# Performance work log

Hardware: AMD Instinct MI355X
Metric: run time of the kernel (lower is better)

Reference implementation:

```python
import jax, jax.numpy as jnp
import numpy as np

N_SRC = 100000
E = 300000
D = 256
HEADS = 8
D_K = D // HEADS
N_EXPERTS = 5


def setup_inputs() -> dict:
    key = jax.random.key(0)
    kx, ki, ke, kw, kb = jax.random.split(key, 5)
    x = jax.random.normal(kx, (N_SRC, D), dtype=jnp.float32)
    index = jax.random.randint(ki, (E,), 0, N_SRC)
    # disjoint routing masks: each output row handled by exactly one of 5 linears
    expert_id = jax.random.randint(ke, (E,), 0, N_EXPERTS)
    masks = expert_id[None, :] == jnp.arange(N_EXPERTS)[:, None]  # [5, E] bool
    # learned params: 5 independent Linear(D, D) layers (torch layout: y = x @ W.T + b)
    bound = 1.0 / np.sqrt(D)
    W = jax.random.uniform(kw, (N_EXPERTS, D, D), minval=-bound, maxval=bound, dtype=jnp.float32)
    b = jax.random.uniform(kb, (N_EXPERTS, D), minval=-bound, maxval=bound, dtype=jnp.float32)
    return {"x": x, "W": W, "b": b, "index": index, "masks": masks}


def reference(x, W, b, index, masks):
    # gather source rows for every output slot: [E, D]
    xi = x[index]
    out = jnp.zeros((xi.shape[0], D), dtype=x.dtype)
    # sequential masked overwrite matches torch's output[mask] = ... semantics
    for i in range(N_EXPERTS):
        yi = xi @ W[i].T + b[i]  # [E, D]
        out = jnp.where(masks[i][:, None], yi, out)
    return out.reshape(xi.shape[0], HEADS, D_K)
```

## Files before the change

kernel.cpp:

```cpp
#include <hip/hip_runtime.h>
#include <hip/hip_bf16.h>

#define E_TOT   300000
#define D_DIM   256
#define N_EXP   5
#define BM      64
#define LDK     264
#define NB_CNT  ((E_TOT + 255) / 256)
#define MAX_TILES (E_TOT / BM + N_EXP)
#define CHUNK   8
#define NCHUNK  ((NB_CNT + CHUNK - 1) / CHUNK)

typedef __attribute__((ext_vector_type(8))) short bf16x8;
typedef __attribute__((ext_vector_type(4))) float f32x4;

__device__ inline unsigned short f2bf(float f) {
  union { float f; unsigned u; } v; v.f = f;
  unsigned u = v.u;
  u += 0x7FFFu + ((u >> 16) & 1u);
  return (unsigned short)(u >> 16);
}

__global__ void detect_kernel(const unsigned int* __restrict__ m32, int* __restrict__ hdr) {
  int tid = blockIdx.x * blockDim.x + threadIdx.x;
  const int n = (N_EXP * E_TOT) / 4;
  unsigned s = 0;
  for (int i = tid; i < n; i += gridDim.x * blockDim.x) {
    unsigned v = m32[i];
    s += (v & 0xFFu) + ((v >> 8) & 0xFFu) + ((v >> 16) & 0xFFu) + ((v >> 24) & 0xFFu);
  }
  for (int o = 32; o > 0; o >>= 1) s += __shfl_down(s, o);
  if ((threadIdx.x & 63) == 0 && s) atomicAdd(&hdr[5], (int)s);
}

__device__ inline int get_expert(const void* masks, int e, bool is_u8) {
  if (is_u8) {
    const unsigned char* m = (const unsigned char*)masks;
#pragma unroll
    for (int i = 0; i < N_EXP; ++i) if (m[(size_t)i * E_TOT + e]) return i;
  } else {
    const int* m = (const int*)masks;
#pragma unroll
    for (int i = 0; i < N_EXP; ++i) if (m[(size_t)i * E_TOT + e]) return i;
  }
  return 0;
}

__global__ void count_kernel(const void* __restrict__ masks, const int* __restrict__ hdr,
                             int* __restrict__ blockCounts) {
  __shared__ int wc[4][N_EXP];
  bool is_u8 = (hdr[5] == E_TOT);
  int e = blockIdx.x * blockDim.x + threadIdx.x;
  int ex = (e < E_TOT) ? get_expert(masks, e, is_u8) : -1;
  int w = threadIdx.x >> 6, lane = threadIdx.x & 63;
#pragma unroll
  for (int i = 0; i < N_EXP; ++i) {
    unsigned long long bal = __ballot(ex == i);
    if (lane == 0) wc[w][i] = __popcll(bal);
  }
  __syncthreads();
  if (threadIdx.x < N_EXP)
    blockCounts[blockIdx.x * N_EXP + threadIdx.x] =
        wc[0][threadIdx.x] + wc[1][threadIdx.x] + wc[2][threadIdx.x] + wc[3][threadIdx.x];
}

__global__ void scan_kernel(const int* __restrict__ blockCounts, int* __restrict__ hdr,
                            int* __restrict__ blockBase) {
  __shared__ int cs[NCHUNK][N_EXP];
  __shared__ int cp[NCHUNK][N_EXP];
  int t = threadIdx.x;
  if (t < NCHUNK) {
    int s[N_EXP] = {0, 0, 0, 0, 0};
    int b1 = min((t + 1) * CHUNK, NB_CNT);
    for (int b = t * CHUNK; b < b1; ++b)
#pragma unroll
      for (int i = 0; i < N_EXP; ++i) s[i] += blockCounts[b * N_EXP + i];
#pragma unroll
    for (int i = 0; i < N_EXP; ++i) cs[t][i] = s[i];
  }
  __syncthreads();
  if (t < N_EXP) {
    int run = 0;
    for (int c = 0; c < NCHUNK; ++c) { cp[c][t] = run; run += cs[c][t]; }
    hdr[t] = run;
  }
  __syncthreads();
  if (t == 0) {
    int run = 0;
    for (int i = 0; i < N_EXP; ++i) { hdr[8 + i] = run; run += hdr[i]; }
  }
  __syncthreads();
  if (t < NCHUNK) {
    int r[N_EXP];
#pragma unroll
    for (int i = 0; i < N_EXP; ++i) r[i] = hdr[8 + i] + cp[t][i];
    int b1 = min((t + 1) * CHUNK, NB_CNT);
    for (int b = t * CHUNK; b < b1; ++b)
#pragma unroll
      for (int i = 0; i < N_EXP; ++i) { blockBase[b * N_EXP + i] = r[i]; r[i] += blockCounts[b * N_EXP + i]; }
  }
}

__global__ void scatter_kernel(const void* __restrict__ masks, const int* __restrict__ hdr,
                               const int* __restrict__ blockBase, int* __restrict__ perm) {
  __shared__ int wc[4][N_EXP];
  __shared__ int wo[4][N_EXP];
  __shared__ int bb[N_EXP];
  bool is_u8 = (hdr[5] == E_TOT);
  int e = blockIdx.x * blockDim.x + threadIdx.x;
  int ex = (e < E_TOT) ? get_expert(masks, e, is_u8) : -1;
  int w = threadIdx.x >> 6, lane = threadIdx.x & 63;
  unsigned long long myBal = 0;
#pragma unroll
  for (int i = 0; i < N_EXP; ++i) {
    unsigned long long bal = __ballot(ex == i);
    if (lane == 0) wc[w][i] = __popcll(bal);
    if (ex == i) myBal = bal;
  }
  if (threadIdx.x < N_EXP) bb[threadIdx.x] = blockBase[blockIdx.x * N_EXP + threadIdx.x];
  __syncthreads();
  if (threadIdx.x < 4 * N_EXP) {
    int ww = threadIdx.x / N_EXP, ii = threadIdx.x % N_EXP;
    int s = 0;
    for (int p = 0; p < ww; ++p) s += wc[p][ii];
    wo[ww][ii] = s;
  }
  __syncthreads();
  if (ex >= 0) {
    int rank = __popcll(myBal & ((1ull << lane) - 1ull));
    perm[bb[ex] + wo[w][ex] + rank] = e;
  }
}

__global__ void convw_kernel(const float* __restrict__ W, unsigned short* __restrict__ Wbf) {
  int i = blockIdx.x * blockDim.x + threadIdx.x;
  float4 v = ((const float4*)W)[i];
  ushort4 o;
  o.x = f2bf(v.x); o.y = f2bf(v.y); o.z = f2bf(v.z); o.w = f2bf(v.w);
  ((ushort4*)Wbf)[i] = o;
}

template <bool PRE>
__launch_bounds__(256, 4)
__global__ void gemm_kernel(const float* __restrict__ x, const float* __restrict__ W,
                            const unsigned short* __restrict__ Wbf,
                            const float* __restrict__ bias, const int* __restrict__ index,
                            const int* __restrict__ hdr, const int* __restrict__ perm,
                            float* __restrict__ out) {
  __shared__ __align__(16) unsigned short lA[BM * LDK];
  __shared__ int srcRow[BM];
  __shared__ int outRow[BM];

  int t = (int)blockIdx.x;
  int ex = -1, trow = 0, cnt = 0, accT = 0;
#pragma unroll
  for (int i = 0; i < N_EXP; ++i) {
    int c = hdr[i];
    int nt = (c + BM - 1) / BM;
    if (ex < 0 && t < accT + nt) { ex = i; trow = t - accT; cnt = c; }
    accT += nt;
  }
  if (ex < 0) return;
  int row0 = hdr[8 + ex] + trow * BM;
  int rows = min(BM, cnt - trow * BM);

  const int tt = threadIdx.x;
  if (tt < BM) {
    int rr = min(tt, rows - 1);
    int e = perm[row0 + rr];
    outRow[tt] = e;
    srcRow[tt] = index[e];
  }
  __syncthreads();

#pragma unroll
  for (int i = 0; i < 16; ++i) {
    int lin = i * 256 + tt;
    int r = lin >> 6;
    int c4 = lin & 63;
    const float4 v = ((const float4*)(x + (size_t)srcRow[r] * D_DIM))[c4];
    ushort4 o;
    o.x = f2bf(v.x); o.y = f2bf(v.y); o.z = f2bf(v.z); o.w = f2bf(v.w);
    *(ushort4*)&lA[r * LDK + c4 * 4] = o;
  }
  __syncthreads();

  const int w = tt >> 6, lane = tt & 63, quad = lane >> 4, l16 = lane & 15;

  f32x4 acc[4][4];
#pragma unroll
  for (int mt = 0; mt < 4; ++mt)
#pragma unroll
    for (int nt = 0; nt < 4; ++nt) acc[mt][nt] = (f32x4){0.f, 0.f, 0.f, 0.f};

#pragma unroll
  for (int ks = 0; ks < 8; ++ks) {
    int k0 = ks * 32 + quad * 8;
    bf16x8 a[4], b[4];
#pragma unroll
    for (int mt = 0; mt < 4; ++mt)
      a[mt] = *(const bf16x8*)&lA[(mt * 16 + l16) * LDK + k0];
#pragma unroll
    for (int nt = 0; nt < 4; ++nt) {
      int col = w * 64 + nt * 16 + l16;
      if (PRE) {
        b[nt] = *(const bf16x8*)&Wbf[((size_t)ex * D_DIM + col) * D_DIM + k0];
      } else {
        const float* wp = W + ((size_t)ex * D_DIM + col) * D_DIM + k0;
        float4 v0 = ((const float4*)wp)[0];
        float4 v1 = ((const float4*)wp)[1];
        bf16x8 bb;
        bb[0] = (short)f2bf(v0.x); bb[1] = (short)f2bf(v0.y);
        bb[2] = (short)f2bf(v0.z); bb[3] = (short)f2bf(v0.w);
        bb[4] = (short)f2bf(v1.x); bb[5] = (short)f2bf(v1.y);
        bb[6] = (short)f2bf(v1.z); bb[7] = (short)f2bf(v1.w);
        b[nt] = bb;
      }
    }
#pragma unroll
    for (int mt = 0; mt < 4; ++mt)
#pragma unroll
      for (int nt = 0; nt < 4; ++nt)
        acc[mt][nt] = __builtin_amdgcn_mfma_f32_16x16x32_bf16(a[mt], b[nt], acc[mt][nt], 0, 0, 0);
  }

#pragma unroll
  for (int nt = 0; nt < 4; ++nt) {
    int col = w * 64 + nt * 16 + l16;
    float bv = bias[ex * D_DIM + col];
#pragma unroll
    for (int mt = 0; mt < 4; ++mt) {
#pragma unroll
      for (int r = 0; r < 4; ++r) {
        int rl = mt * 16 + quad * 4 + r;
        if (rl < rows)
          out[(size_t)outRow[rl] * D_DIM + col] = acc[mt][nt][r] + bv;
      }
    }
  }
}

extern "C" void kernel_launch(void* const* d_in, const int* in_sizes, int n_in,
                              void* d_out, int out_size, void* d_ws, size_t ws_size,
                              hipStream_t stream) {
  const float* x     = (const float*)d_in[0];
  const float* W     = (const float*)d_in[1];
  const float* bias  = (const float*)d_in[2];
  const int*   index = (const int*)d_in[3];
  const void*  masks = d_in[4];
  float* out = (float*)d_out;

  int* hdr = (int*)d_ws;
  const size_t wbfB  = (size_t)N_EXP * D_DIM * D_DIM * 2;
  const size_t permB = (size_t)E_TOT * 4;
  const size_t bcB   = (size_t)NB_CNT * N_EXP * 4;

  bool pre = (ws_size >= 1024 + wbfB + permB + 2 * bcB);
  size_t off = 1024;
  unsigned short* Wbf = nullptr;
  if (pre) { Wbf = (unsigned short*)((char*)d_ws + off); off += wbfB; }
  int* perm = (int*)((char*)d_ws + off); off += permB;
  int* bc   = (int*)((char*)d_ws + off); off += bcB;
  int* bb   = (int*)((char*)d_ws + off);

  hipMemsetAsync(d_ws, 0, 1024, stream);
  detect_kernel<<<256, 256, 0, stream>>>((const unsigned int*)masks, hdr);
  count_kernel<<<NB_CNT, 256, 0, stream>>>(masks, hdr, bc);
  scan_kernel<<<1, 256, 0, stream>>>(bc, hdr, bb);
  if (pre) convw_kernel<<<(N_EXP * D_DIM * D_DIM / 4 + 255) / 256, 256, 0, stream>>>(W, Wbf);
  scatter_kernel<<<NB_CNT, 256, 0, stream>>>(masks, hdr, bb, perm);
  if (pre)
    gemm_kernel<true><<<MAX_TILES, 256, 0, stream>>>(x, W, Wbf, bias, index, hdr, perm, out);
  else
    gemm_kernel<false><<<MAX_TILES, 256, 0, stream>>>(x, W, Wbf, bias, index, hdr, perm, out);
}
```

Measured before the change: 548.4 us.

## Fuse mask detection, counting and weight conversion; use atomic cursors; stage output stores

Merges the detect, count and weight-conversion kernels into one prep kernel that checks the mask dtype per block and accumulates expert counts with global atomics. The single-block scan kernel is dropped: scatter now claims per-block offsets with atomic cursors. The GEMM epilogue stages results in shared memory and writes full rows with coalesced nontemporal vector stores. This cuts the number of launches and the serial scan, at the cost of a non-deterministic row order within each expert and a per-block dtype detection heuristic.

```diff
diff --git a/kernel.cpp b/kernel.cpp
--- a/kernel.cpp
+++ b/kernel.cpp
@@ -1,15 +1,13 @@
 #include <hip/hip_runtime.h>
-#include <hip/hip_bf16.h>
 
 #define E_TOT   300000
 #define D_DIM   256
 #define N_EXP   5
 #define BM      64
 #define LDK     264
+#define LDF     260
 #define NB_CNT  ((E_TOT + 255) / 256)
 #define MAX_TILES (E_TOT / BM + N_EXP)
-#define CHUNK   8
-#define NCHUNK  ((NB_CNT + CHUNK - 1) / CHUNK)
 
 typedef __attribute__((ext_vector_type(8))) short bf16x8;
 typedef __attribute__((ext_vector_type(4))) float f32x4;
@@ -21,18 +19,6 @@
   return (unsigned short)(u >> 16);
 }
 
-__global__ void detect_kernel(const unsigned int* __restrict__ m32, int* __restrict__ hdr) {
-  int tid = blockIdx.x * blockDim.x + threadIdx.x;
-  const int n = (N_EXP * E_TOT) / 4;
-  unsigned s = 0;
-  for (int i = tid; i < n; i += gridDim.x * blockDim.x) {
-    unsigned v = m32[i];
-    s += (v & 0xFFu) + ((v >> 8) & 0xFFu) + ((v >> 16) & 0xFFu) + ((v >> 24) & 0xFFu);
-  }
-  for (int o = 32; o > 0; o >>= 1) s += __shfl_down(s, o);
-  if ((threadIdx.x & 63) == 0 && s) atomicAdd(&hdr[5], (int)s);
-}
-
 __device__ inline int get_expert(const void* masks, int e, bool is_u8) {
   if (is_u8) {
     const unsigned char* m = (const unsigned char*)masks;
@@ -46,70 +32,62 @@
   return 0;
 }
 
-__global__ void count_kernel(const void* __restrict__ masks, const int* __restrict__ hdr,
-                             int* __restrict__ blockCounts) {
+__global__ void prep_kernel(const float* __restrict__ W, unsigned short* __restrict__ Wbf,
+                            const void* __restrict__ masks, int* __restrict__ hdr,
+                            int doConv) {
   __shared__ int wc[4][N_EXP];
-  bool is_u8 = (hdr[5] == E_TOT);
-  int e = blockIdx.x * blockDim.x + threadIdx.x;
-  int ex = (e < E_TOT) ? get_expert(masks, e, is_u8) : -1;
-  int w = threadIdx.x >> 6, lane = threadIdx.x & 63;
+  __shared__ int s_u8ok;
+  const int tt = threadIdx.x, w = tt >> 6, lane = tt & 63;
+  const int gtid = (int)blockIdx.x * 256 + tt;
+
+  const unsigned char* m8 = (const unsigned char*)masks;
+  int cnt1 = 1, ex = -1;
+  if (gtid < E_TOT) {
+    cnt1 = 0; int exu = 0;
+#pragma unroll
+    for (int i = 0; i < N_EXP; ++i) {
+      int tb = (m8[(size_t)i * E_TOT + gtid] != 0);
+      cnt1 += tb; if (tb) exu = i;
+    }
+    ex = exu;
+  }
+  if (tt == 0) s_u8ok = 1;
+  __syncthreads();
+  if (cnt1 != 1) s_u8ok = 0;
+  __syncthreads();
+  const int is_u8 = s_u8ok;
+  if (!is_u8 && gtid < E_TOT) ex = get_expert(masks, gtid, false);
+
 #pragma unroll
   for (int i = 0; i < N_EXP; ++i) {
     unsigned long long bal = __ballot(ex == i);
     if (lane == 0) wc[w][i] = __popcll(bal);
   }
-  __syncthreads();
-  if (threadIdx.x < N_EXP)
-    blockCounts[blockIdx.x * N_EXP + threadIdx.x] =
-        wc[0][threadIdx.x] + wc[1][threadIdx.x] + wc[2][threadIdx.x] + wc[3][threadIdx.x];
-}
-
-__global__ void scan_kernel(const int* __restrict__ blockCounts, int* __restrict__ hdr,
-                            int* __restrict__ blockBase) {
-  __shared__ int cs[NCHUNK][N_EXP];
-  __shared__ int cp[NCHUNK][N_EXP];
-  int t = threadIdx.x;
-  if (t < NCHUNK) {
-    int s[N_EXP] = {0, 0, 0, 0, 0};
-    int b1 = min((t + 1) * CHUNK, NB_CNT);
-    for (int b = t * CHUNK; b < b1; ++b)
-#pragma unroll
-      for (int i = 0; i < N_EXP; ++i) s[i] += blockCounts[b * N_EXP + i];
-#pragma unroll
-    for (int i = 0; i < N_EXP; ++i) cs[t][i] = s[i];
-  }
-  __syncthreads();
-  if (t < N_EXP) {
-    int run = 0;
-    for (int c = 0; c < NCHUNK; ++c) { cp[c][t] = run; run += cs[c][t]; }
-    hdr[t] = run;
-  }
-  __syncthreads();
-  if (t == 0) {
-    int run = 0;
-    for (int i = 0; i < N_EXP; ++i) { hdr[8 + i] = run; run += hdr[i]; }
-  }
-  __syncthreads();
-  if (t < NCHUNK) {
-    int r[N_EXP];
-#pragma unroll
-    for (int i = 0; i < N_EXP; ++i) r[i] = hdr[8 + i] + cp[t][i];
-    int b1 = min((t + 1) * CHUNK, NB_CNT);
-    for (int b = t * CHUNK; b < b1; ++b)
-#pragma unroll
-      for (int i = 0; i < N_EXP; ++i) { blockBase[b * N_EXP + i] = r[i]; r[i] += blockCounts[b * N_EXP + i]; }
-  }
+  if (doConv) {
+    const int n4 = (N_EXP * D_DIM * D_DIM) / 4;
+    for (int i = gtid; i < n4; i += (int)gridDim.x * 256) {
+      float4 v = ((const float4*)W)[i];
+      ushort4 o4;
+      o4.x = f2bf(v.x); o4.y = f2bf(v.y); o4.z = f2bf(v.z); o4.w = f2bf(v.w);
+      ((ushort4*)Wbf)[i] = o4;
+    }
+  }
+  __syncthreads();
+  if (tt < N_EXP)
+    atomicAdd(&hdr[tt], wc[0][tt] + wc[1][tt] + wc[2][tt] + wc[3][tt]);
+  if (tt == 0 && blockIdx.x == 0) hdr[6] = is_u8;
 }
 
 __global__ void scatter_kernel(const void* __restrict__ masks, const int* __restrict__ hdr,
-                               const int* __restrict__ blockBase, int* __restrict__ perm) {
+                               int* __restrict__ cursor, int* __restrict__ perm) {
   __shared__ int wc[4][N_EXP];
   __shared__ int wo[4][N_EXP];
   __shared__ int bb[N_EXP];
-  bool is_u8 = (hdr[5] == E_TOT);
-  int e = blockIdx.x * blockDim.x + threadIdx.x;
+  const int tt = threadIdx.x, w = tt >> 6, lane = tt & 63;
+  const int e = (int)blockIdx.x * 256 + tt;
+  const bool is_u8 = (hdr[6] != 0);
+
   int ex = (e < E_TOT) ? get_expert(masks, e, is_u8) : -1;
-  int w = threadIdx.x >> 6, lane = threadIdx.x & 63;
   unsigned long long myBal = 0;
 #pragma unroll
   for (int i = 0; i < N_EXP; ++i) {
@@ -117,27 +95,25 @@
     if (lane == 0) wc[w][i] = __popcll(bal);
     if (ex == i) myBal = bal;
   }
-  if (threadIdx.x < N_EXP) bb[threadIdx.x] = blockBase[blockIdx.x * N_EXP + threadIdx.x];
-  __syncthreads();
-  if (threadIdx.x < 4 * N_EXP) {
-    int ww = threadIdx.x / N_EXP, ii = threadIdx.x % N_EXP;
+  __syncthreads();
+  if (tt < 4 * N_EXP) {
+    int ww = tt / N_EXP, ii = tt % N_EXP;
     int s = 0;
     for (int p = 0; p < ww; ++p) s += wc[p][ii];
     wo[ww][ii] = s;
   }
+  if (tt < N_EXP) {
+    int tot = wc[0][tt] + wc[1][tt] + wc[2][tt] + wc[3][tt];
+    int old = atomicAdd(&cursor[tt], tot);
+    int base = 0;
+    for (int i = 0; i < tt; ++i) base += hdr[i];
+    bb[tt] = base + old;
+  }
   __syncthreads();
   if (ex >= 0) {
     int rank = __popcll(myBal & ((1ull << lane) - 1ull));
     perm[bb[ex] + wo[w][ex] + rank] = e;
   }
-}
-
-__global__ void convw_kernel(const float* __restrict__ W, unsigned short* __restrict__ Wbf) {
-  int i = blockIdx.x * blockDim.x + threadIdx.x;
-  float4 v = ((const float4*)W)[i];
-  ushort4 o;
-  o.x = f2bf(v.x); o.y = f2bf(v.y); o.z = f2bf(v.z); o.w = f2bf(v.w);
-  ((ushort4*)Wbf)[i] = o;
 }
 
 template <bool PRE>
@@ -152,16 +128,17 @@
   __shared__ int outRow[BM];
 
   int t = (int)blockIdx.x;
-  int ex = -1, trow = 0, cnt = 0, accT = 0;
+  int ex = -1, trow = 0, cnt = 0, accT = 0, base = 0, run = 0;
 #pragma unroll
   for (int i = 0; i < N_EXP; ++i) {
     int c = hdr[i];
     int nt = (c + BM - 1) / BM;
-    if (ex < 0 && t < accT + nt) { ex = i; trow = t - accT; cnt = c; }
+    if (ex < 0 && t < accT + nt) { ex = i; trow = t - accT; cnt = c; base = run; }
     accT += nt;
+    run += c;
   }
   if (ex < 0) return;
-  int row0 = hdr[8 + ex] + trow * BM;
+  int row0 = base + trow * BM;
   int rows = min(BM, cnt - trow * BM);
 
   const int tt = threadIdx.x;
@@ -176,12 +153,12 @@
 #pragma unroll
   for (int i = 0; i < 16; ++i) {
     int lin = i * 256 + tt;
-    int r = lin >> 6;
+    int rr = lin >> 6;
     int c4 = lin & 63;
-    const float4 v = ((const float4*)(x + (size_t)srcRow[r] * D_DIM))[c4];
-    ushort4 o;
-    o.x = f2bf(v.x); o.y = f2bf(v.y); o.z = f2bf(v.z); o.w = f2bf(v.w);
-    *(ushort4*)&lA[r * LDK + c4 * 4] = o;
+    const float4 v = ((const float4*)(x + (size_t)srcRow[rr] * D_DIM))[c4];
+    ushort4 o4;
+    o4.x = f2bf(v.x); o4.y = f2bf(v.y); o4.z = f2bf(v.z); o4.w = f2bf(v.w);
+    *(ushort4*)&lA[rr * LDK + c4 * 4] = o4;
   }
   __syncthreads();
 
@@ -224,17 +201,37 @@
         acc[mt][nt] = __builtin_amdgcn_mfma_f32_16x16x32_bf16(a[mt], b[nt], acc[mt][nt], 0, 0, 0);
   }
 
-#pragma unroll
-  for (int nt = 0; nt < 4; ++nt) {
-    int col = w * 64 + nt * 16 + l16;
-    float bv = bias[ex * D_DIM + col];
-#pragma unroll
-    for (int mt = 0; mt < 4; ++mt) {
-#pragma unroll
-      for (int r = 0; r < 4; ++r) {
-        int rl = mt * 16 + quad * 4 + r;
-        if (rl < rows)
-          out[(size_t)outRow[rl] * D_DIM + col] = acc[mt][nt][r] + bv;
+  float bv[4];
+#pragma unroll
+  for (int nt = 0; nt < 4; ++nt) bv[nt] = bias[ex * D_DIM + w * 64 + nt * 16 + l16];
+
+  float* lsf = (float*)lA;
+#pragma unroll
+  for (int chunk = 0; chunk < 2; ++chunk) {
+    __syncthreads();
+#pragma unroll
+    for (int mtl = 0; mtl < 2; ++mtl) {
+      int mt = chunk * 2 + mtl;
+#pragma unroll
+      for (int nt = 0; nt < 4; ++nt) {
+        int col = w * 64 + nt * 16 + l16;
+#pragma unroll
+        for (int r = 0; r < 4; ++r) {
+          int lr = mtl * 16 + quad * 4 + r;
+          lsf[lr * LDF + col] = acc[mt][nt][r] + bv[nt];
+        }
+      }
+    }
+    __syncthreads();
+    int r8 = tt >> 3, c8 = tt & 7;
+    int grow = chunk * 32 + r8;
+    if (grow < rows) {
+      float* op = out + (size_t)outRow[grow] * D_DIM;
+#pragma unroll
+      for (int j = 0; j < 8; ++j) {
+        int c4 = c8 + j * 8;
+        f32x4 v4 = *(const f32x4*)&lsf[r8 * LDF + c4 * 4];
+        __builtin_nontemporal_store(v4, (f32x4*)(op + c4 * 4));
       }
     }
   }
@@ -253,22 +250,15 @@
   int* hdr = (int*)d_ws;
   const size_t wbfB  = (size_t)N_EXP * D_DIM * D_DIM * 2;
   const size_t permB = (size_t)E_TOT * 4;
-  const size_t bcB   = (size_t)NB_CNT * N_EXP * 4;
-
-  bool pre = (ws_size >= 1024 + wbfB + permB + 2 * bcB);
+  bool pre = (ws_size >= 1024 + wbfB + permB);
   size_t off = 1024;
   unsigned short* Wbf = nullptr;
   if (pre) { Wbf = (unsigned short*)((char*)d_ws + off); off += wbfB; }
-  int* perm = (int*)((char*)d_ws + off); off += permB;
-  int* bc   = (int*)((char*)d_ws + off); off += bcB;
-  int* bb   = (int*)((char*)d_ws + off);
-
-  hipMemsetAsync(d_ws, 0, 1024, stream);
-  detect_kernel<<<256, 256, 0, stream>>>((const unsigned int*)masks, hdr);
-  count_kernel<<<NB_CNT, 256, 0, stream>>>(masks, hdr, bc);
-  scan_kernel<<<1, 256, 0, stream>>>(bc, hdr, bb);
-  if (pre) convw_kernel<<<(N_EXP * D_DIM * D_DIM / 4 + 255) / 256, 256, 0, stream>>>(W, Wbf);
-  scatter_kernel<<<NB_CNT, 256, 0, stream>>>(masks, hdr, bb, perm);
+  int* perm = (int*)((char*)d_ws + off);
+
+  (void)hipMemsetAsync(d_ws, 0, 1024, stream);
+  prep_kernel<<<NB_CNT, 256, 0, stream>>>(W, Wbf, masks, hdr, pre ? 1 : 0);
+  scatter_kernel<<<NB_CNT, 256, 0, stream>>>(masks, hdr, hdr + 16, perm);
   if (pre)
     gemm_kernel<true><<<MAX_TILES, 256, 0, stream>>>(x, W, Wbf, bias, index, hdr, perm, out);
   else
```

Result: faster. 478.5 us (-12.7%).
